# Kernel tuning notes

Measured on AMD Instinct MI355X. Metric: run time of the kernel, lower is better.

## Reference

```python
import jax, jax.numpy as jnp
import numpy as np

B, N, E, H = 4, 1024, 1024, 16
D = E // H

def setup_inputs() -> dict:
    key = jax.random.key(0)
    ks = jax.random.split(key, 5)
    return {
        "x": jax.random.normal(ks[0], (B, N, E), dtype=jnp.float32),
        "Wqkv": jax.random.normal(ks[1], (E, 3 * E), dtype=jnp.float32) * 0.02,
        "bqkv": jax.random.normal(ks[2], (3 * E,), dtype=jnp.float32) * 0.02,
        "Wfc": jax.random.normal(ks[3], (E, E), dtype=jnp.float32) * 0.02,
        "bfc": jax.random.normal(ks[4], (E,), dtype=jnp.float32) * 0.02,
    }

def reference(x, Wqkv, bqkv, Wfc, bfc):
    b, n, e = x.shape
    h, d = H, E // H
    qkv = x @ Wqkv + bqkv                      # [b, n, 3e]
    q, k, v = jnp.split(qkv, 3, axis=-1)       # each [b, n, e]
    # view to [b, n, h, d] then RAW reshape to [b, h, n, d] (faithful to original,
    # which uses .reshape, not transpose — mixes seq/head axes)
    q = q.reshape(b, n, h, d).reshape(b, h, n, d)
    k = k.reshape(b, n, h, d).reshape(b, h, n, d)
    v = v.reshape(b, n, h, d).reshape(b, h, n, d)
    scores = jnp.einsum('bhqd,bhkd->bhqk', q, k) / jnp.sqrt(jnp.float32(d))
    causal = jnp.triu(jnp.ones((n, n), dtype=bool), k=1)  # True above diagonal
    scores = jnp.where(causal, -jnp.inf, scores)
    attn = jax.nn.softmax(scores, axis=-1)
    out = jnp.einsum('bhqk,bhkd->bhqd', attn, v)          # [b, h, n, d]
    # raw reshape back to [b, n, h, d] then flatten heads (faithful)
    out = out.reshape(b, n, h, d).reshape(b, n, e)
    return out @ Wfc + bfc
```

## Files before the change

kernel.cpp:

```cpp
#include <hip/hip_runtime.h>


typedef __bf16 bf16x8 __attribute__((ext_vector_type(8)));
typedef float f32x4 __attribute__((ext_vector_type(4)));

__device__ __forceinline__ unsigned short f2bf(float f) {
    unsigned u = __float_as_uint(f);
    u += 0x7fffu + ((u >> 16) & 1u);
    return (unsigned short)(u >> 16);
}

union FragU { uint4 u; bf16x8 v; };

__device__ __forceinline__ bf16x8 ld_frag(const unsigned short* p) {
    FragU x; x.u = *(const uint4*)p; return x.v;
}

__device__ __forceinline__ void gload_lds16(const void* g, void* l) {
    __builtin_amdgcn_global_load_lds(
        (const __attribute__((address_space(1))) void*)g,
        (__attribute__((address_space(3))) void*)l, 16, 0, 0);
}

__global__ void cvt_bf16(const float* __restrict__ in, unsigned short* __restrict__ out, int n4) {
    int i = blockIdx.x * blockDim.x + threadIdx.x;
    int stride = gridDim.x * blockDim.x;
    for (; i < n4; i += stride) {
        float4 f = ((const float4*)in)[i];
        unsigned a = (unsigned)f2bf(f.x) | ((unsigned)f2bf(f.y) << 16);
        unsigned b = (unsigned)f2bf(f.z) | ((unsigned)f2bf(f.w) << 16);
        ((uint2*)out)[i] = make_uint2(a, b);
    }
}

__global__ void transpose_cvt(const float* __restrict__ W, unsigned short* __restrict__ Wt,
                              int rows, int cols) {
    __shared__ float tile[32][33];
    int c0 = blockIdx.x * 32, r0 = blockIdx.y * 32;
    for (int i = threadIdx.y; i < 32; i += 8)
        tile[i][threadIdx.x] = W[(r0 + i) * cols + c0 + threadIdx.x];
    __syncthreads();
    for (int i = threadIdx.y; i < 32; i += 8)
        Wt[(c0 + i) * (long)rows + r0 + threadIdx.x] = f2bf(tile[threadIdx.x][i]);
}

__global__ void transpose_v(const unsigned short* __restrict__ v,
                            unsigned short* __restrict__ vt) {
    __shared__ unsigned short tile[32][33];
    int bh = blockIdx.z;
    int n0 = blockIdx.x * 32, d0 = blockIdx.y * 32;
    const unsigned short* src = v + (long)bh * 65536;
    unsigned short* dst = vt + (long)bh * 65536;
    for (int i = threadIdx.y; i < 32; i += 8)
        tile[i][threadIdx.x] = src[(n0 + i) * 64 + d0 + threadIdx.x];
    __syncthreads();
    for (int i = threadIdx.y; i < 32; i += 8)
        dst[(d0 + i) * 1024 + n0 + threadIdx.x] = tile[threadIdx.x][i];
}

template <int MODE>
__global__ __launch_bounds__(256) void gemm128(
    const unsigned short* __restrict__ A,
    const unsigned short* __restrict__ Bt,
    const float* __restrict__ bias,
    unsigned short* __restrict__ qb,
    unsigned short* __restrict__ kb,
    unsigned short* __restrict__ vb,
    float* __restrict__ outf)
{
    const int K = 1024;
    __shared__ unsigned short As[2][4096];
    __shared__ unsigned short Bs[2][4096];
    int t = threadIdx.x, lane = t & 63, w = t >> 6;
    int wm = w >> 1, wn = w & 1;
    int lrow = lane >> 4, lcol = lane & 15;
    int tn0 = blockIdx.x * 128, tm0 = blockIdx.y * 128;

    int seg0 = w * 1024;
    int seg1 = (w + 4) * 1024;
    int off0 = seg0 + lane * 16, off1 = seg1 + lane * 16;
    int r0 = off0 >> 6, cb0 = off0 & 63;
    int r1 = off1 >> 6, cb1 = off1 & 63;

    const char* gA = (const char*)A;
    const char* gB = (const char*)Bt;

    f32x4 acc[4][4] = {};

    auto STAGE = [&](int buf, int kt) {
        long kby = (long)kt * 2;
        gload_lds16(gA + (long)(tm0 + r0) * 2048 + kby + cb0, (char*)&As[buf][0] + seg0);
        gload_lds16(gA + (long)(tm0 + r1) * 2048 + kby + cb1, (char*)&As[buf][0] + seg1);
        gload_lds16(gB + (long)(tn0 + r0) * 2048 + kby + cb0, (char*)&Bs[buf][0] + seg0);
        gload_lds16(gB + (long)(tn0 + r1) * 2048 + kby + cb1, (char*)&Bs[buf][0] + seg1);
    };

    STAGE(0, 0);
    asm volatile("s_waitcnt vmcnt(0)");
    __syncthreads();

    int cur = 0;
    for (int kt = 0; kt < K; kt += 32) {
        if (kt + 32 < K) STAGE(cur ^ 1, kt + 32);

        bf16x8 af[4], bfr[4];
        #pragma unroll
        for (int mi = 0; mi < 4; ++mi)
            af[mi] = ld_frag(&As[cur][0] + (wm * 64 + mi * 16 + lcol) * 32 + lrow * 8);
        #pragma unroll
        for (int ni = 0; ni < 4; ++ni)
            bfr[ni] = ld_frag(&Bs[cur][0] + (wn * 64 + ni * 16 + lcol) * 32 + lrow * 8);
        #pragma unroll
        for (int mi = 0; mi < 4; ++mi)
            #pragma unroll
            for (int ni = 0; ni < 4; ++ni)
                acc[mi][ni] = __builtin_amdgcn_mfma_f32_16x16x32_bf16(af[mi], bfr[ni], acc[mi][ni], 0, 0, 0);

        __syncthreads();
        cur ^= 1;
    }

    #pragma unroll
    for (int mi = 0; mi < 4; ++mi) {
        int gr0 = tm0 + wm * 64 + mi * 16 + lrow * 4;
        #pragma unroll
        for (int ni = 0; ni < 4; ++ni) {
            int gc = tn0 + wn * 64 + ni * 16 + lcol;
            float bv = bias[gc];
            if (MODE == 0) {
                int sec = gc >> 10, ei = gc & 1023;
                unsigned short* dst = sec == 0 ? qb : (sec == 1 ? kb : vb);
                #pragma unroll
                for (int r = 0; r < 4; ++r)
                    dst[(long)(gr0 + r) * 1024 + ei] = f2bf(acc[mi][ni][r] + bv);
            } else {
                #pragma unroll
                for (int r = 0; r < 4; ++r)
                    outf[(long)(gr0 + r) * 1024 + gc] = acc[mi][ni][r] + bv;
            }
        }
    }
}

__global__ __launch_bounds__(256) void attn(
    const unsigned short* __restrict__ qbuf,
    const unsigned short* __restrict__ kbuf,
    const unsigned short* __restrict__ vtbuf,
    unsigned short* __restrict__ obuf)
{
    __shared__ char smem[4 * 32 * 68 * 4 + 512 + 512] __attribute__((aligned(16)));
    unsigned short (*Ps)[32][40] = (unsigned short (*)[32][40])smem;
    float* accS = (float*)smem;
    float* mS = (float*)(smem + 4 * 32 * 68 * 4);
    float* lS = mS + 128;

    int bh = blockIdx.y, j = blockIdx.x;
    const unsigned short* Q  = qbuf + (long)bh * 65536;
    const unsigned short* Kp = kbuf + (long)bh * 65536;
    const unsigned short* VT = vtbuf + (long)bh * 65536;
    unsigned short* O = obuf + (long)bh * 65536;
    int t = threadIdx.x, lane = t & 63, w = t >> 6;
    int lrow = lane >> 4, lcol = lane & 15;
    const float NEG = -__builtin_inff();

    #pragma unroll
    for (int pass = 0; pass < 2; ++pass) {
        int qt = pass == 0 ? j : 31 - j;
        int qbase = qt * 32;
        int T = qt + 1;

        bf16x8 qf[2][2];
        #pragma unroll
        for (int qg = 0; qg < 2; ++qg)
            #pragma unroll
            for (int kc = 0; kc < 2; ++kc)
                qf[qg][kc] = ld_frag(Q + (long)(qbase + qg * 16 + lcol) * 64 + kc * 32 + lrow * 8);

        f32x4 acc[2][4] = {};
        float m_i[2] = {NEG, NEG}, l_i[2] = {0.f, 0.f};

        if (w < T) {
            int kt = w * 32;
            bf16x8 kf[2][2];
            #pragma unroll
            for (int kg = 0; kg < 2; ++kg)
                #pragma unroll
                for (int kc = 0; kc < 2; ++kc)
                    kf[kg][kc] = ld_frag(Kp + (long)(kt + kg * 16 + lcol) * 64 + kc * 32 + lrow * 8);

            for (;; kt += 128) {
                f32x4 s[2][2] = {};
                __builtin_amdgcn_s_setprio(1);
                #pragma unroll
                for (int kg = 0; kg < 2; ++kg)
                    #pragma unroll
                    for (int kc = 0; kc < 2; ++kc) {
                        s[0][kg] = __builtin_amdgcn_mfma_f32_16x16x32_bf16(kf[kg][kc], qf[0][kc], s[0][kg], 0, 0, 0);
                        s[1][kg] = __builtin_amdgcn_mfma_f32_16x16x32_bf16(kf[kg][kc], qf[1][kc], s[1][kg], 0, 0, 0);
                    }
                __builtin_amdgcn_s_setprio(0);

                bool more = kt + 128 < T * 32;
                bf16x8 kn[2][2];
                if (more) {
                    #pragma unroll
                    for (int kg = 0; kg < 2; ++kg)
                        #pragma unroll
                        for (int kc = 0; kc < 2; ++kc)
                            kn[kg][kc] = ld_frag(Kp + (long)(kt + 128 + kg * 16 + lcol) * 64 + kc * 32 + lrow * 8);
                }
                bf16x8 vf[4];
                #pragma unroll
                for (int dg = 0; dg < 4; ++dg)
                    vf[dg] = ld_frag(VT + (long)(dg * 16 + lcol) * 1024 + kt + lrow * 8);

                #pragma unroll
                for (int qg = 0; qg < 2; ++qg) {
                    int q = qbase + qg * 16 + lcol;
                    float tv[8];
                    float mx = NEG;
                    #pragma unroll
                    for (int kg = 0; kg < 2; ++kg)
                        #pragma unroll
                        for (int r = 0; r < 4; ++r) {
                            int kglob = kt + kg * 16 + lrow * 4 + r;
                            float v = s[qg][kg][r] * 0.125f;
                            tv[kg * 4 + r] = kglob > q ? NEG : v;
                            mx = fmaxf(mx, tv[kg * 4 + r]);
                        }
                    mx = fmaxf(mx, __shfl_xor(mx, 16));
                    mx = fmaxf(mx, __shfl_xor(mx, 32));
                    float mnew = fmaxf(m_i[qg], mx);
                    float alpha = __expf(m_i[qg] - mnew);
                    float p[8], ps = 0.f;
                    #pragma unroll
                    for (int jj = 0; jj < 8; ++jj) { p[jj] = __expf(tv[jj] - mnew); ps += p[jj]; }
                    #pragma unroll
                    for (int kg = 0; kg < 2; ++kg) {
                        ushort4 pk;
                        pk.x = f2bf(p[kg * 4 + 0]); pk.y = f2bf(p[kg * 4 + 1]);
                        pk.z = f2bf(p[kg * 4 + 2]); pk.w = f2bf(p[kg * 4 + 3]);
                        *(ushort4*)&Ps[w][qg * 16 + lcol][kg * 16 + lrow * 4] = pk;
                    }
                    ps += __shfl_xor(ps, 16);
                    ps += __shfl_xor(ps, 32);
                    l_i[qg] = l_i[qg] * alpha + ps;
                    m_i[qg] = mnew;
                    #pragma unroll
                    for (int dg = 0; dg < 4; ++dg)
                        #pragma unroll
                        for (int r = 0; r < 4; ++r)
                            acc[qg][dg][r] *= alpha;
                }

                bf16x8 pb[2];
                pb[0] = ld_frag(&Ps[w][lcol][lrow * 8]);
                pb[1] = ld_frag(&Ps[w][16 + lcol][lrow * 8]);
                __builtin_amdgcn_s_setprio(1);
                #pragma unroll
                for (int dg = 0; dg < 4; ++dg) {
                    acc[0][dg] = __builtin_amdgcn_mfma_f32_16x16x32_bf16(vf[dg], pb[0], acc[0][dg], 0, 0, 0);
                    acc[1][dg] = __builtin_amdgcn_mfma_f32_16x16x32_bf16(vf[dg], pb[1], acc[1][dg], 0, 0, 0);
                }
                __builtin_amdgcn_s_setprio(0);

                if (!more) break;
                #pragma unroll
                for (int kg = 0; kg < 2; ++kg)
                    #pragma unroll
                    for (int kc = 0; kc < 2; ++kc)
                        kf[kg][kc] = kn[kg][kc];
            }
        }

        __syncthreads();
        #pragma unroll
        for (int qg = 0; qg < 2; ++qg) {
            int q = qg * 16 + lcol;
            if (lrow == 0) { mS[w * 32 + q] = m_i[qg]; lS[w * 32 + q] = l_i[qg]; }
            #pragma unroll
            for (int dg = 0; dg < 4; ++dg)
                *(f32x4*)&accS[(w * 32 + q) * 68 + dg * 16 + lrow * 4] = acc[qg][dg];
        }
        __syncthreads();

        {
            int qq = t >> 3, d0 = (t & 7) * 8;
            float m0 = mS[qq], m1 = mS[32 + qq], m2 = mS[64 + qq], m3 = mS[96 + qq];
            float M = fmaxf(fmaxf(m0, m1), fmaxf(m2, m3));
            float e0 = __expf(m0 - M), e1 = __expf(m1 - M), e2 = __expf(m2 - M), e3 = __expf(m3 - M);
            float L = e0 * lS[qq] + e1 * lS[32 + qq] + e2 * lS[64 + qq] + e3 * lS[96 + qq];
            float inv = 1.f / L;
            const float* a0 = &accS[qq * 68 + d0];
            const float* a1 = &accS[(32 + qq) * 68 + d0];
            const float* a2 = &accS[(64 + qq) * 68 + d0];
            const float* a3 = &accS[(96 + qq) * 68 + d0];
            unsigned short h[8];
            #pragma unroll
            for (int jj = 0; jj < 8; ++jj)
                h[jj] = f2bf((e0 * a0[jj] + e1 * a1[jj] + e2 * a2[jj] + e3 * a3[jj]) * inv);
            uint4 pk;
            pk.x = (unsigned)h[0] | ((unsigned)h[1] << 16);
            pk.y = (unsigned)h[2] | ((unsigned)h[3] << 16);
            pk.z = (unsigned)h[4] | ((unsigned)h[5] << 16);
            pk.w = (unsigned)h[6] | ((unsigned)h[7] << 16);
            *(uint4*)&O[(long)(qbase + qq) * 64 + d0] = pk;
        }
        __syncthreads();
    }
}

extern "C" void kernel_launch(void* const* d_in, const int* in_sizes, int n_in,
                              void* d_out, int out_size, void* d_ws, size_t ws_size,
                              hipStream_t stream) {
    const float* x    = (const float*)d_in[0];
    const float* Wqkv = (const float*)d_in[1];
    const float* bqkv = (const float*)d_in[2];
    const float* Wfc  = (const float*)d_in[3];
    const float* bfc  = (const float*)d_in[4];
    float* out = (float*)d_out;

    unsigned short* ws    = (unsigned short*)d_ws;
    unsigned short* xb    = ws;
    unsigned short* wqkvT = xb + (4u << 20);
    unsigned short* wfcT  = wqkvT + (3u << 20);
    unsigned short* qb    = wfcT + (1u << 20);
    unsigned short* kb    = qb + (4u << 20);
    unsigned short* vb    = kb + (4u << 20);
    unsigned short* vbT   = xb;
    unsigned short* ob    = vb;

    cvt_bf16<<<dim3(2048), dim3(256), 0, stream>>>(x, xb, (4 << 20) / 4);
    transpose_cvt<<<dim3(3072 / 32, 1024 / 32), dim3(32, 8), 0, stream>>>(Wqkv, wqkvT, 1024, 3072);
    transpose_cvt<<<dim3(1024 / 32, 1024 / 32), dim3(32, 8), 0, stream>>>(Wfc, wfcT, 1024, 1024);

    gemm128<0><<<dim3(24, 32), dim3(256), 0, stream>>>(xb, wqkvT, bqkv, qb, kb, vb, nullptr);
    transpose_v<<<dim3(32, 2, 64), dim3(32, 8), 0, stream>>>(vb, vbT);
    attn<<<dim3(16, 64), dim3(256), 0, stream>>>(qb, kb, vbT, ob);
    gemm128<1><<<dim3(8, 32), dim3(256), 0, stream>>>(ob, wfcT, bfc, nullptr, nullptr, nullptr, out);
}
```

Baseline: 121.3 us.

## Skip lazy softmax rescaling in attention and remap blocks across XCDs

Adds a lazy online-softmax rescale: the running max and accumulator rescaling are skipped when every lane's new tile max exceeds the stored max by at most 8, tracked with a wave-wide vote. This removes the per-tile alpha exponentials and the accumulator multiplies in most iterations, at the cost of a branch and p values bounded by up to e^8 before the bf16 conversion. The attention grid is also flattened to 1D, with block IDs remapped so all query tiles of one batch-head land on the same XCD for L2 reuse of K/V.

After: 120.9 us. About the same (-0.3%).

```diff
diff --git a/kernel.cpp b/kernel.cpp
--- a/kernel.cpp
+++ b/kernel.cpp
@@ -154,7 +154,11 @@
     float* mS = (float*)(smem + 4 * 32 * 68 * 4);
     float* lS = mS + 128;
 
-    int bh = blockIdx.y, j = blockIdx.x;
+    int id = blockIdx.x;
+    int xcd = id & 7, slot = id >> 3;
+    int bh = xcd + 8 * (slot >> 4);
+    int j = slot & 15;
+
     const unsigned short* Q  = qbuf + (long)bh * 65536;
     const unsigned short* Kp = kbuf + (long)bh * 65536;
     const unsigned short* VT = vtbuf + (long)bh * 65536;
@@ -214,10 +218,10 @@
                 for (int dg = 0; dg < 4; ++dg)
                     vf[dg] = ld_frag(VT + (long)(dg * 16 + lcol) * 1024 + kt + lrow * 8);
 
+                float tv[2][8], pmax[2];
                 #pragma unroll
                 for (int qg = 0; qg < 2; ++qg) {
                     int q = qbase + qg * 16 + lcol;
-                    float tv[8];
                     float mx = NEG;
                     #pragma unroll
                     for (int kg = 0; kg < 2; ++kg)
@@ -225,16 +229,35 @@
                         for (int r = 0; r < 4; ++r) {
                             int kglob = kt + kg * 16 + lrow * 4 + r;
                             float v = s[qg][kg][r] * 0.125f;
-                            tv[kg * 4 + r] = kglob > q ? NEG : v;
-                            mx = fmaxf(mx, tv[kg * 4 + r]);
+                            tv[qg][kg * 4 + r] = kglob > q ? NEG : v;
+                            mx = fmaxf(mx, tv[qg][kg * 4 + r]);
                         }
                     mx = fmaxf(mx, __shfl_xor(mx, 16));
                     mx = fmaxf(mx, __shfl_xor(mx, 32));
-                    float mnew = fmaxf(m_i[qg], mx);
-                    float alpha = __expf(m_i[qg] - mnew);
+                    pmax[qg] = mx;
+                }
+                float alpha[2] = {1.f, 1.f};
+                bool small = (pmax[0] - m_i[0] <= 8.f) && (pmax[1] - m_i[1] <= 8.f);
+                if (!__all(small)) {
+                    #pragma unroll
+                    for (int qg = 0; qg < 2; ++qg) {
+                        float mnew = fmaxf(m_i[qg], pmax[qg]);
+                        alpha[qg] = __expf(m_i[qg] - mnew);
+                        m_i[qg] = mnew;
+                    }
+                    #pragma unroll
+                    for (int qg = 0; qg < 2; ++qg)
+                        #pragma unroll
+                        for (int dg = 0; dg < 4; ++dg)
+                            #pragma unroll
+                            for (int r = 0; r < 4; ++r)
+                                acc[qg][dg][r] *= alpha[qg];
+                }
+                #pragma unroll
+                for (int qg = 0; qg < 2; ++qg) {
                     float p[8], ps = 0.f;
                     #pragma unroll
-                    for (int jj = 0; jj < 8; ++jj) { p[jj] = __expf(tv[jj] - mnew); ps += p[jj]; }
+                    for (int jj = 0; jj < 8; ++jj) { p[jj] = __expf(tv[qg][jj] - m_i[qg]); ps += p[jj]; }
                     #pragma unroll
                     for (int kg = 0; kg < 2; ++kg) {
                         ushort4 pk;
@@ -244,13 +267,7 @@
                     }
                     ps += __shfl_xor(ps, 16);
                     ps += __shfl_xor(ps, 32);
-                    l_i[qg] = l_i[qg] * alpha + ps;
-                    m_i[qg] = mnew;
-                    #pragma unroll
-                    for (int dg = 0; dg < 4; ++dg)
-                        #pragma unroll
-                        for (int r = 0; r < 4; ++r)
-                            acc[qg][dg][r] *= alpha;
+                    l_i[qg] = l_i[qg] * alpha[qg] + ps;
                 }
 
                 bf16x8 pb[2];
@@ -336,6 +353,6 @@
 
     gemm128<0><<<dim3(24, 32), dim3(256), 0, stream>>>(xb, wqkvT, bqkv, qb, kb, vb, nullptr);
     transpose_v<<<dim3(32, 2, 64), dim3(32, 8), 0, stream>>>(vb, vbT);
-    attn<<<dim3(16, 64), dim3(256), 0, stream>>>(qb, kb, vbT, ob);
+    attn<<<dim3(1024), dim3(256), 0, stream>>>(qb, kb, vbT, ob);
     gemm128<1><<<dim3(8, 32), dim3(256), 0, stream>>>(ob, wfcT, bfc, nullptr, nullptr, nullptr, out);
 }
```
